# Kernel optimization log

Measured on AMD Instinct MI355X. Metric: run time of the kernel, lower is better.

The kernel has to match this reference:

```python
import jax, jax.numpy as jnp
import numpy as np

N, E, H, R = 20000, 400000, 128, 20


def setup_inputs() -> dict:
    key = jax.random.key(0)
    ks = jax.random.split(key, 12)
    inv_h = 1.0 / np.sqrt(H)
    inv_r = 1.0 / np.sqrt(R)
    return {
        "s": jax.random.normal(ks[0], (N, H), jnp.float32),
        "v": jax.random.normal(ks[1], (N, 3, H), jnp.float32),
        "edge_rbf": jax.random.normal(ks[2], (E, R), jnp.float32),
        "edge_cutoff": jax.random.uniform(ks[3], (E,), jnp.float32),
        "edge_vec": jax.random.normal(ks[4], (E, 3), jnp.float32),
        "W1": jax.random.normal(ks[5], (H, H), jnp.float32) * inv_h,
        "b1": jnp.zeros((H,), jnp.float32),
        "W2": jax.random.normal(ks[6], (H, 3 * H), jnp.float32) * inv_h,
        "b2": jnp.zeros((3 * H,), jnp.float32),
        "Wr": jax.random.normal(ks[7], (R, 3 * H), jnp.float32) * inv_r,
        "br": jnp.zeros((3 * H,), jnp.float32),
        "edge_index": jax.random.randint(ks[8], (2, E), 0, N, jnp.int64),
    }


def reference(s, v, edge_rbf, edge_cutoff, edge_vec, W1, b1, W2, b2, Wr, br, edge_index):
    i, j = edge_index[0], edge_index[1]
    n = s.shape[0]
    # rbf projection modulated by cutoff: [E, 3H]
    W = (edge_rbf @ Wr + br) * edge_cutoff[:, None]
    # scalar MLP on gathered source features: [E, 3H]
    h = jax.nn.silu(s[j] @ W1 + b1)
    x = (h @ W2 + b2) * W
    x_ss, x_sv, x_vv = jnp.split(x, 3, axis=-1)  # each [E, H]
    ds = jax.ops.segment_sum(x_ss, i, num_segments=n)
    # dv1: outer product of edge direction with gated scalars -> [E,3,H]
    dv1 = jax.ops.segment_sum(x_sv[:, None, :] * edge_vec[:, :, None], i, num_segments=n)
    # equivariant term: project v_j onto edge direction, re-expand
    inner = jnp.sum(v[j] * edge_vec[:, :, None], axis=1)  # [E, H]
    dv2 = jax.ops.segment_sum((inner * x_vv)[:, None, :] * edge_vec[:, :, None], i, num_segments=n)
    return ds, dv1 + dv2
```

## Files before the change

kernel.cpp:

```cpp
#include <hip/hip_runtime.h>
#include <hip/hip_bf16.h>

#define HDIM 128
#define H3   384
#define RDIM 20
#define NPB  16
#define NPR  4
#define CHNK 32
#define RBLK 512

typedef unsigned short u16;
typedef unsigned int   u32;

__device__ __forceinline__ u16 f2bf(float f) {
    __hip_bfloat16 h = __float2bfloat16(f);
    return *(u16*)&h;
}
__device__ __forceinline__ float bflo(u32 u) {
    union { u32 i; float f; } x; x.i = u << 16; return x.f;
}
__device__ __forceinline__ float bfhi(u32 u) {
    union { u32 i; float f; } x; x.i = u & 0xffff0000u; return x.f;
}
__device__ __forceinline__ u32 pk(float lo, float hi) {
    return (u32)f2bf(lo) | ((u32)f2bf(hi) << 16);
}

__global__ __launch_bounds__(128) void node_mlp_kernel(
    const float* __restrict__ s, const float* __restrict__ W1,
    const float* __restrict__ b1, const float* __restrict__ W2,
    const float* __restrict__ b2, const float* __restrict__ v,
    u32* __restrict__ P3, int N)
{
    __shared__ float sS[NPB][HDIM];
    __shared__ float sH[NPB][HDIM];
    const int t  = threadIdx.x;
    const int n0 = blockIdx.x * NPB;

    #pragma unroll
    for (int n = 0; n < NPB; ++n) {
        int node = n0 + n;
        sS[n][t] = (node < N) ? s[(size_t)node * HDIM + t] : 0.f;
    }
    __syncthreads();

    float acc[NPB];
    #pragma unroll
    for (int n = 0; n < NPB; ++n) acc[n] = 0.f;
    for (int k = 0; k < HDIM; ++k) {
        float w = W1[k * HDIM + t];
        #pragma unroll
        for (int n = 0; n < NPB; ++n) acc[n] += sS[n][k] * w;
    }
    float bb = b1[t];
    #pragma unroll
    for (int n = 0; n < NPB; ++n) {
        float z = acc[n] + bb;
        sH[n][t] = z / (1.f + __expf(-z));
    }
    __syncthreads();

    float a0[NPB], a1[NPB], a2[NPB];
    #pragma unroll
    for (int n = 0; n < NPB; ++n) { a0[n] = 0.f; a1[n] = 0.f; a2[n] = 0.f; }
    for (int k2 = 0; k2 < HDIM / 2; ++k2) {
        float2 hv[NPB];
        #pragma unroll
        for (int n = 0; n < NPB; ++n) hv[n] = ((const float2*)sH[n])[k2];
        #pragma unroll
        for (int kk = 0; kk < 2; ++kk) {
            int k = 2 * k2 + kk;
            float w0 = W2[k * H3 + t];
            float w1 = W2[k * H3 + t + 128];
            float w2 = W2[k * H3 + t + 256];
            #pragma unroll
            for (int n = 0; n < NPB; ++n) {
                float h = kk ? hv[n].y : hv[n].x;
                a0[n] += h * w0;
                a1[n] += h * w1;
                a2[n] += h * w2;
            }
        }
    }
    float c0 = b2[t], c1 = b2[t + 128], c2 = b2[t + 256];
    #pragma unroll
    for (int n = 0; n < NPB; ++n) {
        int node = n0 + n;
        if (node < N) {
            size_t vb = (size_t)node * H3;
            float vx = v[vb + t], vy = v[vb + 128 + t], vz = v[vb + 256 + t];
            size_t pb = (size_t)node * H3 + t;
            P3[pb]       = pk(a0[n] + c0, a1[n] + c1);
            P3[pb + 128] = pk(a2[n] + c2, vx);
            P3[pb + 256] = pk(vy, vz);
        }
    }
}

__global__ void hist_kernel(const int* __restrict__ eidx, int* __restrict__ counts, int E)
{
    int e = blockIdx.x * 256 + threadIdx.x;
    if (e < E) atomicAdd(&counts[eidx[e]], 1);
}

__global__ __launch_bounds__(1024) void scan_kernel(
    const int* __restrict__ counts, int* __restrict__ rstart,
    int* __restrict__ cursor, int N)
{
    __shared__ int part[1024];
    const int t = threadIdx.x;
    const int C = 20;
    int loc[C];
    int s = 0;
    #pragma unroll
    for (int q = 0; q < C; ++q) {
        int idx = t * C + q;
        int c = (idx < N) ? counts[idx] : 0;
        loc[q] = s; s += c;
    }
    part[t] = s;
    __syncthreads();
    for (int off = 1; off < 1024; off <<= 1) {
        int vv = (t >= off) ? part[t - off] : 0;
        __syncthreads();
        part[t] += vv;
        __syncthreads();
    }
    int boff = (t > 0) ? part[t - 1] : 0;
    #pragma unroll
    for (int q = 0; q < C; ++q) {
        int idx = t * C + q;
        if (idx < N) {
            int st = boff + loc[q];
            rstart[idx] = st;
            cursor[idx] = st;
        }
    }
    if (t == 1023) rstart[N] = part[1023];
}

__global__ void scatter_kernel(const int* __restrict__ eidx, int* __restrict__ cursor,
                               int* __restrict__ eord, int E)
{
    int e = blockIdx.x * 256 + threadIdx.x;
    if (e < E) {
        int i = eidx[e];
        int pos = atomicAdd(&cursor[i], 1);
        eord[pos] = e;
    }
}

__global__ __launch_bounds__(RBLK) void reduce_kernel(
    const int* __restrict__ rstart, const int* __restrict__ eord,
    const float* __restrict__ rbf, const float* __restrict__ cutoff,
    const float* __restrict__ evec, const float* __restrict__ Wr,
    const float* __restrict__ br, const u32* __restrict__ P3,
    const int* __restrict__ eidx, float* __restrict__ ds,
    float* __restrict__ dv, int E, int N)
{
    const int t  = threadIdx.x;
    const int ch = t & (HDIM - 1);
    const int u  = t >> 7;

    float wr0[RDIM], wr1[RDIM], wr2[RDIM];
    #pragma unroll
    for (int k = 0; k < RDIM; ++k) {
        wr0[k] = Wr[k * H3 + ch];
        wr1[k] = Wr[k * H3 + ch + 128];
        wr2[k] = Wr[k * H3 + ch + 256];
    }
    const float br0 = br[ch], br1 = br[ch + 128], br2 = br[ch + 256];

    __shared__ int   sJoff[CHNK];
    __shared__ float sCut[CHNK], sVx[CHNK], sVy[CHNK], sVz[CHNK];
    __shared__ __attribute__((aligned(16))) float sRbf[CHNK][RDIM];
    __shared__ float sRed[3][4][HDIM];

    for (int nn = 0; nn < NPR; ++nn) {
        int node = blockIdx.x * NPR + nn;
        if (node >= N) break;
        int beg = rstart[node], end = rstart[node + 1];
        float accs = 0.f, accx = 0.f, accy = 0.f, accz = 0.f;

        for (int c0 = beg; c0 < end; c0 += CHNK) {
            int cnt = min(CHNK, end - c0);
            __syncthreads();
            if (t < cnt) {
                int e = eord[c0 + t];
                sJoff[t] = eidx[E + e] * H3;
                sCut[t]  = cutoff[e];
                sVx[t]   = evec[3 * e];
                sVy[t]   = evec[3 * e + 1];
                sVz[t]   = evec[3 * e + 2];
            }
            for (int x = t; x < cnt * RDIM; x += RBLK) {
                int n = x / RDIM, k = x - n * RDIM;
                int e = eord[c0 + n];
                sRbf[n][k] = rbf[(size_t)e * RDIM + k];
            }
            __syncthreads();

            int q = u;
            u32 ca = 0, cb = 0, cc = 0;
            if (q < cnt) {
                int idx = sJoff[q] + ch;
                ca = P3[idx]; cb = P3[idx + 128]; cc = P3[idx + 256];
            }
            for (; q < cnt; q += 4) {
                int qn = q + 4;
                u32 na = 0, nb = 0, nc = 0;
                if (qn < cnt) {
                    int idx = sJoff[qn] + ch;
                    na = P3[idx]; nb = P3[idx + 128]; nc = P3[idx + 256];
                }
                const float4* r4 = (const float4*)sRbf[q];
                float w0 = 0.f, w1 = 0.f, w2 = 0.f;
                #pragma unroll
                for (int k4 = 0; k4 < 5; ++k4) {
                    float4 r = r4[k4];
                    w0 += r.x * wr0[4*k4] + r.y * wr0[4*k4+1] + r.z * wr0[4*k4+2] + r.w * wr0[4*k4+3];
                    w1 += r.x * wr1[4*k4] + r.y * wr1[4*k4+1] + r.z * wr1[4*k4+2] + r.w * wr1[4*k4+3];
                    w2 += r.x * wr2[4*k4] + r.y * wr2[4*k4+1] + r.z * wr2[4*k4+2] + r.w * wr2[4*k4+3];
                }
                float cu = sCut[q];
                float ex = sVx[q], ey = sVy[q], ez = sVz[q];
                float pss = bflo(ca), psv = bfhi(ca);
                float pvv = bflo(cb), vx  = bfhi(cb);
                float vy  = bflo(cc), vz  = bfhi(cc);
                float xss = (w0 + br0) * cu * pss;
                float xsv = (w1 + br1) * cu * psv;
                float xvv = (w2 + br2) * cu * pvv;
                float inner = vx * ex + vy * ey + vz * ez;
                float coef  = xsv + inner * xvv;
                accs += xss;
                accx += coef * ex;
                accy += coef * ey;
                accz += coef * ez;
                ca = na; cb = nb; cc = nc;
            }
        }

        __syncthreads();
        if (u > 0) {
            sRed[u - 1][0][ch] = accs;
            sRed[u - 1][1][ch] = accx;
            sRed[u - 1][2][ch] = accy;
            sRed[u - 1][3][ch] = accz;
        }
        __syncthreads();
        if (u == 0) {
            accs += sRed[0][0][ch] + sRed[1][0][ch] + sRed[2][0][ch];
            accx += sRed[0][1][ch] + sRed[1][1][ch] + sRed[2][1][ch];
            accy += sRed[0][2][ch] + sRed[1][2][ch] + sRed[2][2][ch];
            accz += sRed[0][3][ch] + sRed[1][3][ch] + sRed[2][3][ch];
            ds[(size_t)node * HDIM + ch] = accs;
            size_t dvi = (size_t)node * H3;
            dv[dvi + ch]       = accx;
            dv[dvi + 128 + ch] = accy;
            dv[dvi + 256 + ch] = accz;
        }
    }
}

extern "C" void kernel_launch(void* const* d_in, const int* in_sizes, int n_in,
                              void* d_out, int out_size, void* d_ws, size_t ws_size,
                              hipStream_t stream)
{
    const float* s    = (const float*)d_in[0];
    const float* v    = (const float*)d_in[1];
    const float* rbf  = (const float*)d_in[2];
    const float* cut  = (const float*)d_in[3];
    const float* evec = (const float*)d_in[4];
    const float* W1   = (const float*)d_in[5];
    const float* b1   = (const float*)d_in[6];
    const float* W2   = (const float*)d_in[7];
    const float* b2   = (const float*)d_in[8];
    const float* Wr   = (const float*)d_in[9];
    const float* br   = (const float*)d_in[10];
    const int*   eidx = (const int*)d_in[11];

    const int N = in_sizes[0] / HDIM;
    const int E = in_sizes[3];

    float* out = (float*)d_out;
    float* ds  = out;
    float* dv  = out + (size_t)N * HDIM;

    char* w = (char*)d_ws;
    u32* P3 = (u32*)w;                     w += ((size_t)N * H3 * 4 + 255) / 256 * 256;
    int* counts = (int*)w;                 w += ((size_t)N * 4 + 255) / 256 * 256;
    int* rstart = (int*)w;                 w += ((size_t)(N + 1) * 4 + 255) / 256 * 256;
    int* cursor = (int*)w;                 w += ((size_t)N * 4 + 255) / 256 * 256;
    int* eord   = (int*)w;

    hipMemsetAsync(counts, 0, (size_t)N * sizeof(int), stream);

    node_mlp_kernel<<<(N + NPB - 1) / NPB, 128, 0, stream>>>(s, W1, b1, W2, b2, v, P3, N);
    hist_kernel<<<(E + 255) / 256, 256, 0, stream>>>(eidx, counts, E);
    scan_kernel<<<1, 1024, 0, stream>>>(counts, rstart, cursor, N);
    scatter_kernel<<<(E + 255) / 256, 256, 0, stream>>>(eidx, cursor, eord, E);
    reduce_kernel<<<(N + NPR - 1) / NPR, RBLK, 0, stream>>>(rstart, eord, rbf, cut, evec,
                                                            Wr, br, P3, eidx, ds, dv, E, N);
}
```

Before: 346.7 us.

## Replace per-node segment reduction with edge-chunk streaming and atomic flushes

The per-node reduction kernel, which gave each node a 512-thread block and combined partial sums through shared memory, is replaced by a kernel that handles fixed 64-edge chunks of the destination-sorted edge list per 128-thread block. Each block accumulates while the destination stays the same and flushes with atomicAdd when it changes. The output is zeroed with a memset first. This is meant to balance work across blocks regardless of node degree and remove the shared-memory reduction and its barriers, at the cost of atomic traffic at chunk and segment boundaries and an extra memset.

```diff
diff --git a/kernel.cpp b/kernel.cpp
--- a/kernel.cpp
+++ b/kernel.cpp
@@ -5,9 +5,7 @@
 #define H3   384
 #define RDIM 20
 #define NPB  16
-#define NPR  4
-#define CHNK 32
-#define RBLK 512
+#define EPB  64
 
 typedef unsigned short u16;
 typedef unsigned int   u32;
@@ -150,116 +148,100 @@
     }
 }
 
-__global__ __launch_bounds__(RBLK) void reduce_kernel(
-    const int* __restrict__ rstart, const int* __restrict__ eord,
+__global__ __launch_bounds__(128, 4) void edge_stream_kernel(
+    const int* __restrict__ eord, const int* __restrict__ eidx,
     const float* __restrict__ rbf, const float* __restrict__ cutoff,
     const float* __restrict__ evec, const float* __restrict__ Wr,
     const float* __restrict__ br, const u32* __restrict__ P3,
-    const int* __restrict__ eidx, float* __restrict__ ds,
-    float* __restrict__ dv, int E, int N)
-{
-    const int t  = threadIdx.x;
-    const int ch = t & (HDIM - 1);
-    const int u  = t >> 7;
+    float* __restrict__ ds, float* __restrict__ dv, int E)
+{
+    const int t    = threadIdx.x;
+    const int base = blockIdx.x * EPB;
+    const int cnt  = min(EPB, E - base);
 
     float wr0[RDIM], wr1[RDIM], wr2[RDIM];
     #pragma unroll
     for (int k = 0; k < RDIM; ++k) {
-        wr0[k] = Wr[k * H3 + ch];
-        wr1[k] = Wr[k * H3 + ch + 128];
-        wr2[k] = Wr[k * H3 + ch + 256];
-    }
-    const float br0 = br[ch], br1 = br[ch + 128], br2 = br[ch + 256];
-
-    __shared__ int   sJoff[CHNK];
-    __shared__ float sCut[CHNK], sVx[CHNK], sVy[CHNK], sVz[CHNK];
-    __shared__ __attribute__((aligned(16))) float sRbf[CHNK][RDIM];
-    __shared__ float sRed[3][4][HDIM];
-
-    for (int nn = 0; nn < NPR; ++nn) {
-        int node = blockIdx.x * NPR + nn;
-        if (node >= N) break;
-        int beg = rstart[node], end = rstart[node + 1];
-        float accs = 0.f, accx = 0.f, accy = 0.f, accz = 0.f;
-
-        for (int c0 = beg; c0 < end; c0 += CHNK) {
-            int cnt = min(CHNK, end - c0);
-            __syncthreads();
-            if (t < cnt) {
-                int e = eord[c0 + t];
-                sJoff[t] = eidx[E + e] * H3;
-                sCut[t]  = cutoff[e];
-                sVx[t]   = evec[3 * e];
-                sVy[t]   = evec[3 * e + 1];
-                sVz[t]   = evec[3 * e + 2];
-            }
-            for (int x = t; x < cnt * RDIM; x += RBLK) {
-                int n = x / RDIM, k = x - n * RDIM;
-                int e = eord[c0 + n];
-                sRbf[n][k] = rbf[(size_t)e * RDIM + k];
-            }
-            __syncthreads();
-
-            int q = u;
-            u32 ca = 0, cb = 0, cc = 0;
-            if (q < cnt) {
-                int idx = sJoff[q] + ch;
-                ca = P3[idx]; cb = P3[idx + 128]; cc = P3[idx + 256];
-            }
-            for (; q < cnt; q += 4) {
-                int qn = q + 4;
-                u32 na = 0, nb = 0, nc = 0;
-                if (qn < cnt) {
-                    int idx = sJoff[qn] + ch;
-                    na = P3[idx]; nb = P3[idx + 128]; nc = P3[idx + 256];
-                }
-                const float4* r4 = (const float4*)sRbf[q];
-                float w0 = 0.f, w1 = 0.f, w2 = 0.f;
-                #pragma unroll
-                for (int k4 = 0; k4 < 5; ++k4) {
-                    float4 r = r4[k4];
-                    w0 += r.x * wr0[4*k4] + r.y * wr0[4*k4+1] + r.z * wr0[4*k4+2] + r.w * wr0[4*k4+3];
-                    w1 += r.x * wr1[4*k4] + r.y * wr1[4*k4+1] + r.z * wr1[4*k4+2] + r.w * wr1[4*k4+3];
-                    w2 += r.x * wr2[4*k4] + r.y * wr2[4*k4+1] + r.z * wr2[4*k4+2] + r.w * wr2[4*k4+3];
-                }
-                float cu = sCut[q];
-                float ex = sVx[q], ey = sVy[q], ez = sVz[q];
-                float pss = bflo(ca), psv = bfhi(ca);
-                float pvv = bflo(cb), vx  = bfhi(cb);
-                float vy  = bflo(cc), vz  = bfhi(cc);
-                float xss = (w0 + br0) * cu * pss;
-                float xsv = (w1 + br1) * cu * psv;
-                float xvv = (w2 + br2) * cu * pvv;
-                float inner = vx * ex + vy * ey + vz * ez;
-                float coef  = xsv + inner * xvv;
-                accs += xss;
-                accx += coef * ex;
-                accy += coef * ey;
-                accz += coef * ez;
-                ca = na; cb = nb; cc = nc;
-            }
-        }
-
-        __syncthreads();
-        if (u > 0) {
-            sRed[u - 1][0][ch] = accs;
-            sRed[u - 1][1][ch] = accx;
-            sRed[u - 1][2][ch] = accy;
-            sRed[u - 1][3][ch] = accz;
-        }
-        __syncthreads();
-        if (u == 0) {
-            accs += sRed[0][0][ch] + sRed[1][0][ch] + sRed[2][0][ch];
-            accx += sRed[0][1][ch] + sRed[1][1][ch] + sRed[2][1][ch];
-            accy += sRed[0][2][ch] + sRed[1][2][ch] + sRed[2][2][ch];
-            accz += sRed[0][3][ch] + sRed[1][3][ch] + sRed[2][3][ch];
-            ds[(size_t)node * HDIM + ch] = accs;
-            size_t dvi = (size_t)node * H3;
-            dv[dvi + ch]       = accx;
-            dv[dvi + 128 + ch] = accy;
-            dv[dvi + 256 + ch] = accz;
-        }
-    }
+        wr0[k] = Wr[k * H3 + t];
+        wr1[k] = Wr[k * H3 + t + 128];
+        wr2[k] = Wr[k * H3 + t + 256];
+    }
+    const float br0 = br[t], br1 = br[t + 128], br2 = br[t + 256];
+
+    __shared__ int   sI[EPB], sJ[EPB];
+    __shared__ float sCut[EPB], sVx[EPB], sVy[EPB], sVz[EPB];
+    __shared__ __attribute__((aligned(16))) float sRbf[EPB][RDIM];
+
+    if (t < cnt) {
+        int e   = eord[base + t];
+        sI[t]   = eidx[e];
+        sJ[t]   = eidx[E + e] * H3;
+        sCut[t] = cutoff[e];
+        sVx[t]  = evec[3 * e];
+        sVy[t]  = evec[3 * e + 1];
+        sVz[t]  = evec[3 * e + 2];
+    }
+    for (int x = t; x < cnt * RDIM; x += 128) {
+        int n = x / RDIM, k = x - n * RDIM;
+        int e = eord[base + n];
+        sRbf[n][k] = rbf[(size_t)e * RDIM + k];
+    }
+    __syncthreads();
+
+    u32 ca, cb, cc;
+    {
+        int idx = sJ[0] + t;
+        ca = P3[idx]; cb = P3[idx + 128]; cc = P3[idx + 256];
+    }
+    int   cur  = sI[0];
+    float accs = 0.f, accx = 0.f, accy = 0.f, accz = 0.f;
+
+    for (int q = 0; q < cnt; ++q) {
+        u32 na = 0, nb = 0, nc = 0;
+        if (q + 1 < cnt) {
+            int idx = sJ[q + 1] + t;
+            na = P3[idx]; nb = P3[idx + 128]; nc = P3[idx + 256];
+        }
+        int iq = sI[q];
+        if (iq != cur) {
+            atomicAdd(&ds[(size_t)cur * HDIM + t], accs);
+            size_t dvi = (size_t)cur * H3;
+            atomicAdd(&dv[dvi + t],       accx);
+            atomicAdd(&dv[dvi + 128 + t], accy);
+            atomicAdd(&dv[dvi + 256 + t], accz);
+            accs = accx = accy = accz = 0.f;
+            cur = iq;
+        }
+        const float4* r4 = (const float4*)sRbf[q];
+        float w0 = 0.f, w1 = 0.f, w2 = 0.f;
+        #pragma unroll
+        for (int k4 = 0; k4 < 5; ++k4) {
+            float4 r = r4[k4];
+            w0 += r.x * wr0[4*k4] + r.y * wr0[4*k4+1] + r.z * wr0[4*k4+2] + r.w * wr0[4*k4+3];
+            w1 += r.x * wr1[4*k4] + r.y * wr1[4*k4+1] + r.z * wr1[4*k4+2] + r.w * wr1[4*k4+3];
+            w2 += r.x * wr2[4*k4] + r.y * wr2[4*k4+1] + r.z * wr2[4*k4+2] + r.w * wr2[4*k4+3];
+        }
+        float cu = sCut[q];
+        float ex = sVx[q], ey = sVy[q], ez = sVz[q];
+        float pss = bflo(ca), psv = bfhi(ca);
+        float pvv = bflo(cb), vx  = bfhi(cb);
+        float vy  = bflo(cc), vz  = bfhi(cc);
+        float xss = (w0 + br0) * cu * pss;
+        float xsv = (w1 + br1) * cu * psv;
+        float xvv = (w2 + br2) * cu * pvv;
+        float inner = vx * ex + vy * ey + vz * ez;
+        float coef  = xsv + inner * xvv;
+        accs += xss;
+        accx += coef * ex;
+        accy += coef * ey;
+        accz += coef * ez;
+        ca = na; cb = nb; cc = nc;
+    }
+    atomicAdd(&ds[(size_t)cur * HDIM + t], accs);
+    size_t dvi = (size_t)cur * H3;
+    atomicAdd(&dv[dvi + t],       accx);
+    atomicAdd(&dv[dvi + 128 + t], accy);
+    atomicAdd(&dv[dvi + 256 + t], accz);
 }
 
 extern "C" void kernel_launch(void* const* d_in, const int* in_sizes, int n_in,
@@ -293,12 +275,14 @@
     int* cursor = (int*)w;                 w += ((size_t)N * 4 + 255) / 256 * 256;
     int* eord   = (int*)w;
 
+    hipMemsetAsync(d_out, 0, (size_t)out_size * sizeof(float), stream);
     hipMemsetAsync(counts, 0, (size_t)N * sizeof(int), stream);
 
     node_mlp_kernel<<<(N + NPB - 1) / NPB, 128, 0, stream>>>(s, W1, b1, W2, b2, v, P3, N);
     hist_kernel<<<(E + 255) / 256, 256, 0, stream>>>(eidx, counts, E);
     scan_kernel<<<1, 1024, 0, stream>>>(counts, rstart, cursor, N);
     scatter_kernel<<<(E + 255) / 256, 256, 0, stream>>>(eidx, cursor, eord, E);
-    reduce_kernel<<<(N + NPR - 1) / NPR, RBLK, 0, stream>>>(rstart, eord, rbf, cut, evec,
-                                                            Wr, br, P3, eidx, ds, dv, E, N);
-}
+    edge_stream_kernel<<<(E + EPB - 1) / EPB, 128, 0, stream>>>(eord, eidx, rbf, cut,
+                                                                evec, Wr, br, P3,
+                                                                ds, dv, E);
+}
```

Measured after the change: 319.8 us. -7.8%, faster.
